# Kernel tuning notes

Measured on AMD Instinct MI355X. Metric: run time of the kernel, lower is better.

The kernel has to match this reference:

```python
import jax, jax.numpy as jnp
import numpy as np

EMBED_DIM = 1024
NUM_HEADS = 16
HEAD_DIM = EMBED_DIM // NUM_HEADS


def setup_inputs() -> dict:
    key = jax.random.key(0)
    ks = jax.random.split(key, 7)
    B, S, D = 2, 2048, EMBED_DIM
    s = 1.0 / np.sqrt(D)
    return {
        "x": jax.random.normal(ks[0], (B, S, D), dtype=jnp.float32),
        "Wq": jax.random.normal(ks[1], (D, D), dtype=jnp.float32) * s,
        "bq": jax.random.normal(ks[2], (D,), dtype=jnp.float32) * 0.01,
        "Wk": jax.random.normal(ks[3], (D, D), dtype=jnp.float32) * s,
        "bk": jax.random.normal(ks[4], (D,), dtype=jnp.float32) * 0.01,
        "Wv": jax.random.normal(ks[5], (D, D), dtype=jnp.float32) * s,
        "bv": jax.random.normal(ks[6], (D,), dtype=jnp.float32) * 0.01,
    }


def reference(x, Wq, bq, Wk, bk, Wv, bv):
    B, S, D = x.shape
    H, Hd = NUM_HEADS, HEAD_DIM
    # QKV projections, then split heads: [B, S, D] -> [B, H, S, Hd]
    q = (x @ Wq + bq).reshape(B, S, H, Hd).transpose(0, 2, 1, 3)
    k = (x @ Wk + bk).reshape(B, S, H, Hd).transpose(0, 2, 1, 3)
    v = (x @ Wv + bv).reshape(B, S, H, Hd).transpose(0, 2, 1, 3)
    # NOTE: the original module applies NO 1/sqrt(head_dim) scaling.
    energy = jnp.einsum("bhqd,bhkd->bhqk", q, k)  # [B, H, S, S]
    attn = jax.nn.softmax(energy, axis=-1)
    out = jnp.einsum("bhqk,bhkd->bhqd", attn, v)
    return out.transpose(0, 2, 1, 3).reshape(B, S, D)
```

## Files before the change

kernel.cpp:

```cpp
#include <hip/hip_runtime.h>
#include <stdint.h>
#include <stddef.h>

typedef _Float16 half_t;
typedef __attribute__((ext_vector_type(8))) _Float16 h16x8;
typedef __attribute__((ext_vector_type(4))) _Float16 h16x4;
typedef __attribute__((ext_vector_type(4))) float f32x4;

#define MFMA16(a, b, c) __builtin_amdgcn_mfma_f32_16x16x32_f16(a, b, c, 0, 0, 0)
#define EXP2(x) __builtin_amdgcn_exp2f(x)

#define SW(row, slot) ((((slot) ^ ((row) & 7))) * 8)

__device__ __forceinline__ void gload_lds16(const half_t* g, half_t* l) {
    __builtin_amdgcn_global_load_lds(
        (const __attribute__((address_space(1))) void*)g,
        (__attribute__((address_space(3))) void*)l, 16, 0, 0);
}

__global__ __launch_bounds__(256) void cvt_x_kernel(const float* __restrict__ x,
                                                    half_t* __restrict__ xh, int n8) {
    int i = blockIdx.x * blockDim.x + threadIdx.x;
    if (i >= n8) return;
    const float4* xv = (const float4*)x;
    float4 a = xv[i * 2 + 0];
    float4 b = xv[i * 2 + 1];
    h16x8 o;
    o[0] = (half_t)a.x; o[1] = (half_t)a.y; o[2] = (half_t)a.z; o[3] = (half_t)a.w;
    o[4] = (half_t)b.x; o[5] = (half_t)b.y; o[6] = (half_t)b.z; o[7] = (half_t)b.w;
    ((h16x8*)xh)[i] = o;
}

__global__ __launch_bounds__(256) void cvt_w_kernel(const float* __restrict__ Wq,
                                                    const float* __restrict__ Wk,
                                                    const float* __restrict__ Wv,
                                                    half_t* __restrict__ Wt) {
    __shared__ float t[32][33];
    const float* W = (blockIdx.z == 0) ? Wq : ((blockIdx.z == 1) ? Wk : Wv);
    int k0 = blockIdx.y * 32, n0 = blockIdx.x * 32;
    int tid = threadIdx.x;
    int r = tid >> 3;
    int c4 = (tid & 7) * 4;
    float4 v = *(const float4*)&W[(size_t)(k0 + r) * 1024 + n0 + c4];
    t[r][c4 + 0] = v.x; t[r][c4 + 1] = v.y; t[r][c4 + 2] = v.z; t[r][c4 + 3] = v.w;
    __syncthreads();
    half_t* o = Wt + (size_t)blockIdx.z * 1024 * 1024 + (size_t)(n0 + r) * 1024 + k0 + c4;
    h16x4 h;
    h[0] = (half_t)t[c4 + 0][r];
    h[1] = (half_t)t[c4 + 1][r];
    h[2] = (half_t)t[c4 + 2][r];
    h[3] = (half_t)t[c4 + 3][r];
    *(h16x4*)o = h;
}

__global__ __launch_bounds__(256, 3) void gemm_qkv_kernel(
    const half_t* __restrict__ xh,
    const half_t* __restrict__ Wt,
    const float* __restrict__ bq, const float* __restrict__ bk,
    const float* __restrict__ bv,
    half_t* __restrict__ qkv)
{
    const int p = blockIdx.z;
    const float* bias = (p == 0) ? bq : ((p == 1) ? bk : bv);
    const half_t* Wp = Wt + (size_t)p * 1024 * 1024;
    const int n0 = blockIdx.x * 128, m0 = blockIdx.y * 128;

    __shared__ half_t Al[128][64];
    __shared__ half_t Bl[128][64];

    const int tid = threadIdx.x;
    const int lane = tid & 63, wid = tid >> 6;
    const int wm = wid >> 1, wn = wid & 1;
    const int g = lane >> 4, r = lane & 15;

    const int lrow = lane >> 3;
    const int swzc = ((lane & 7) ^ lrow) * 8;

    f32x4 acc[4][4];
#pragma unroll
    for (int a = 0; a < 4; a++)
#pragma unroll
        for (int c = 0; c < 4; c++) acc[a][c] = (f32x4){0.f, 0.f, 0.f, 0.f};

    for (int k0 = 0; k0 < 1024; k0 += 64) {
        __syncthreads();
#pragma unroll
        for (int j = 0; j < 4; j++) {
            int issue = wid * 4 + j;
            int row = issue * 8 + lrow;
            gload_lds16(&xh[(size_t)(m0 + row) * 1024 + k0 + swzc], &Al[0][0] + issue * 512);
            gload_lds16(&Wp[(size_t)(n0 + row) * 1024 + k0 + swzc], &Bl[0][0] + issue * 512);
        }
        __syncthreads();

#pragma unroll
        for (int t = 0; t < 2; t++) {
            h16x8 af[4], bf[4];
#pragma unroll
            for (int mi = 0; mi < 4; mi++)
                af[mi] = *(const h16x8*)&Al[wm * 64 + mi * 16 + r][SW(r, t * 4 + g)];
#pragma unroll
            for (int ni = 0; ni < 4; ni++)
                bf[ni] = *(const h16x8*)&Bl[wn * 64 + ni * 16 + r][SW(r, t * 4 + g)];
#pragma unroll
            for (int mi = 0; mi < 4; mi++)
#pragma unroll
                for (int ni = 0; ni < 4; ni++)
                    acc[mi][ni] = MFMA16(af[mi], bf[ni], acc[mi][ni]);
        }
    }

    float bn[4];
#pragma unroll
    for (int ni = 0; ni < 4; ni++) bn[ni] = bias[n0 + wn * 64 + ni * 16 + r];

    if (p == 0) {
        half_t* outp = qkv;
#pragma unroll
        for (int mi = 0; mi < 4; mi++) {
#pragma unroll
            for (int ni = 0; ni < 4; ni++) {
                int n = n0 + wn * 64 + ni * 16 + r;
                int hq = n >> 6, hd = n & 63;
#pragma unroll
                for (int i = 0; i < 4; i++) {
                    int m = m0 + wm * 64 + mi * 16 + g * 4 + i;
                    int b = m >> 11, s = m & 2047;
                    outp[(((size_t)(b * 16 + hq) * 2048 + s) << 6) + hd] =
                        (half_t)(acc[mi][ni][i] + bn[ni]);
                }
            }
        }
    } else if (p == 1) {
        half_t* outp = qkv + (size_t)4194304;
        const int kt = ((m0 & 2047) + wm * 64) >> 6;
        const int bK = (m0 + wm * 64) >> 11;
#pragma unroll
        for (int ni = 0; ni < 4; ni++) {
            int n = n0 + wn * 64 + ni * 16 + r;
            int hK = n >> 6, hd = n & 63;
            int tt = hd >> 5, ggk = (hd >> 3) & 3, jK = hd & 7;
            size_t base = (size_t)(bK * 16 + hK) * 131072 + kt * 4096 + tt * 512 + ggk * 128 + jK;
#pragma unroll
            for (int mi = 0; mi < 4; mi++)
#pragma unroll
                for (int i = 0; i < 4; i++)
                    outp[base + mi * 1024 + (g * 4 + i) * 8] =
                        (half_t)(acc[mi][ni][i] + bn[ni]);
        }
    } else {
        half_t* outp = qkv + (size_t)2 * 4194304;
        const int kt = ((m0 & 2047) + wm * 64) >> 6;
        const int bV = (m0 + wm * 64) >> 11;
        const int hV = (n0 + wn * 64) >> 6;
        size_t base = (size_t)(bV * 16 + hV) * 131072 + kt * 4096 + (g * 16 + r) * 8;
#pragma unroll
        for (int ni = 0; ni < 4; ni++) {
#pragma unroll
            for (int mi = 0; mi < 4; mi++) {
                h16x4 pk;
#pragma unroll
                for (int i = 0; i < 4; i++) pk[i] = (half_t)(acc[mi][ni][i] + bn[ni]);
                *(h16x4*)&outp[base + (ni * 2 + (mi >> 1)) * 512 + (mi & 1) * 4] = pk;
            }
        }
    }
}

__global__ __launch_bounds__(256, 2) void attn_kernel(
    const half_t* __restrict__ Qg,
    const half_t* __restrict__ Kswz,
    const half_t* __restrict__ Vswz,
    float* __restrict__ out)
{
    const int tid = threadIdx.x;
    const int lane = tid & 63;
    const int g = lane >> 4, r = lane & 15;

    const int bid = blockIdx.x;
    const int xcd = bid & 7;
    const int t_  = bid >> 3;
    const int qblk = t_ & 15;
    const int bh = xcd + 8 * (t_ >> 4);

    const int b = bh >> 4, h = bh & 15;
    const half_t* Qb = Qg + (size_t)bh * 131072;
    const half_t* Kp = Kswz + (size_t)bh * 131072;
    const half_t* Vp = Vswz + (size_t)bh * 131072;
    const int q0 = qblk * 128 + (tid >> 6) * 32;
    const int lofs = g * 128 + r * 8;

    h16x8 qf[2][2];
#pragma unroll
    for (int qg = 0; qg < 2; qg++)
#pragma unroll
        for (int t = 0; t < 2; t++) {
            qf[qg][t] = *(const h16x8*)&Qb[(size_t)(q0 + qg * 16 + r) * 64 + t * 32 + g * 8];
            qf[qg][t] *= (half_t)1.44269504f;
        }

    const h16x8 ones8 = {(half_t)1.f, (half_t)1.f, (half_t)1.f, (half_t)1.f,
                         (half_t)1.f, (half_t)1.f, (half_t)1.f, (half_t)1.f};

    f32x4 o[2][4], lsum[2];
#pragma unroll
    for (int qg = 0; qg < 2; qg++) {
#pragma unroll
        for (int d = 0; d < 4; d++) o[qg][d] = (f32x4){0.f, 0.f, 0.f, 0.f};
        lsum[qg] = (f32x4){0.f, 0.f, 0.f, 0.f};
    }
    float m_run[2] = {0.f, 0.f};

    h16x8 kf[8], vf[8];

    auto loadK = [&](int kt) {
#pragma unroll
        for (int kc = 0; kc < 4; kc++)
#pragma unroll
            for (int t = 0; t < 2; t++)
                kf[kc * 2 + t] = *(const h16x8*)&Kp[kt * 4096 + kc * 1024 + t * 512 + lofs];
    };
    auto loadV = [&](int kt) {
#pragma unroll
        for (int dh = 0; dh < 8; dh++)
            vf[dh] = *(const h16x8*)&Vp[kt * 4096 + dh * 512 + lofs];
    };

    auto QKT = [&](f32x4 (&e)[2][4]) {
        __builtin_amdgcn_s_setprio(1);
#pragma unroll
        for (int kc = 0; kc < 4; kc++) {
            e[0][kc] = (f32x4){0.f, 0.f, 0.f, 0.f};
            e[1][kc] = (f32x4){0.f, 0.f, 0.f, 0.f};
#pragma unroll
            for (int t = 0; t < 2; t++) {
                e[0][kc] = MFMA16(kf[kc * 2 + t], qf[0][t], e[0][kc]);
                e[1][kc] = MFMA16(kf[kc * 2 + t], qf[1][t], e[1][kc]);
            }
        }
        __builtin_amdgcn_s_setprio(0);
    };

    auto SOFTMAX_PV = [&](f32x4 (&e)[2][4]) {
        h16x8 pa[2][2];
#pragma unroll
        for (int qg = 0; qg < 2; qg++) {
            float t0 = fmaxf(fmaxf(e[qg][0][0], e[qg][0][1]), e[qg][0][2]);
            float t1 = fmaxf(fmaxf(e[qg][0][3], e[qg][1][0]), e[qg][1][1]);
            float t2 = fmaxf(fmaxf(e[qg][1][2], e[qg][1][3]), e[qg][2][0]);
            float t3 = fmaxf(fmaxf(e[qg][2][1], e[qg][2][2]), e[qg][2][3]);
            float t4 = fmaxf(fmaxf(e[qg][3][0], e[qg][3][1]), e[qg][3][2]);
            float tm = fmaxf(fmaxf(t0, t1), fmaxf(fmaxf(t2, t3), fmaxf(t4, e[qg][3][3])));
            tm = fmaxf(tm, __shfl_xor(tm, 16));
            tm = fmaxf(tm, __shfl_xor(tm, 32));

#pragma unroll
            for (int kc = 0; kc < 4; kc++)
#pragma unroll
                for (int i = 0; i < 4; i++) e[qg][kc][i] = EXP2(e[qg][kc][i] - m_run[qg]);

            if (!__all(tm <= m_run[qg] + 8.f)) {
                float nm = fmaxf(m_run[qg], tm);
                float sc = EXP2(m_run[qg] - nm);
                m_run[qg] = nm;
#pragma unroll
                for (int kc = 0; kc < 4; kc++)
#pragma unroll
                    for (int i = 0; i < 4; i++) e[qg][kc][i] *= sc;
#pragma unroll
                for (int i = 0; i < 4; i++) {
                    float sci = __shfl(sc, (lane & 48) | (g * 4 + i));
                    lsum[qg][i] *= sci;
#pragma unroll
                    for (int d = 0; d < 4; d++) o[qg][d][i] *= sci;
                }
            }

#pragma unroll
            for (int ks = 0; ks < 2; ks++)
#pragma unroll
                for (int hf = 0; hf < 2; hf++)
#pragma unroll
                    for (int i = 0; i < 4; i++)
                        pa[qg][ks][hf * 4 + i] = (half_t)e[qg][ks * 2 + hf][i];
        }

        __builtin_amdgcn_s_setprio(1);
#pragma unroll
        for (int ks = 0; ks < 2; ks++) {
#pragma unroll
            for (int d = 0; d < 4; d++) {
                o[0][d] = MFMA16(pa[0][ks], vf[d * 2 + ks], o[0][d]);
                o[1][d] = MFMA16(pa[1][ks], vf[d * 2 + ks], o[1][d]);
            }
            lsum[0] = MFMA16(pa[0][ks], ones8, lsum[0]);
            lsum[1] = MFMA16(pa[1][ks], ones8, lsum[1]);
        }
        __builtin_amdgcn_s_setprio(0);
    };

    f32x4 eA[2][4], eB[2][4];
    loadK(0);
    QKT(eA);
    loadK(1);

    for (int kt = 0; kt < 32; kt += 2) {
        loadV(kt);
        QKT(eB);
        loadK((kt + 2) & 31);
        SOFTMAX_PV(eA);
        loadV(kt + 1);
        QKT(eA);
        loadK((kt + 3) & 31);
        SOFTMAX_PV(eB);
    }

#pragma unroll
    for (int qg = 0; qg < 2; qg++)
#pragma unroll
        for (int i = 0; i < 4; i++) {
            float inv = 1.0f / lsum[qg][i];
            int s = q0 + qg * 16 + g * 4 + i;
            float* op = out + (size_t)(b * 2048 + s) * 1024 + h * 64 + r;
#pragma unroll
            for (int d = 0; d < 4; d++) op[d * 16] = o[qg][d][i] * inv;
        }
}

extern "C" void kernel_launch(void* const* d_in, const int* in_sizes, int n_in,
                              void* d_out, int out_size, void* d_ws, size_t ws_size,
                              hipStream_t stream) {
    const float* x  = (const float*)d_in[0];
    const float* Wq = (const float*)d_in[1];
    const float* bq = (const float*)d_in[2];
    const float* Wk = (const float*)d_in[3];
    const float* bk = (const float*)d_in[4];
    const float* Wv = (const float*)d_in[5];
    const float* bv = (const float*)d_in[6];
    float* out = (float*)d_out;

    half_t* xh  = (half_t*)d_ws;
    half_t* Wt  = (half_t*)((char*)d_ws + (size_t)8 * 1024 * 1024);
    half_t* qkv = (half_t*)((char*)d_ws + (size_t)14 * 1024 * 1024);
    half_t* Qh  = qkv;
    half_t* Kh  = qkv + (size_t)4194304;
    half_t* Vth = qkv + (size_t)8388608;

    cvt_x_kernel<<<2048, 256, 0, stream>>>(x, xh, 524288);
    cvt_w_kernel<<<dim3(32, 32, 3), 256, 0, stream>>>(Wq, Wk, Wv, Wt);
    gemm_qkv_kernel<<<dim3(8, 32, 3), 256, 0, stream>>>(xh, Wt, bq, bk, bv, qkv);
    attn_kernel<<<512, 256, 0, stream>>>(Qh, Kh, Vth, out);
}
```

Baseline: 99.41 us.

## Halve per-wave query rows in attention and raise occupancy to four blocks

```diff
diff --git a/kernel.cpp b/kernel.cpp
--- a/kernel.cpp
+++ b/kernel.cpp
@@ -167,7 +167,7 @@
     }
 }
 
-__global__ __launch_bounds__(256, 2) void attn_kernel(
+__global__ __launch_bounds__(256, 4) void attn_kernel(
     const half_t* __restrict__ Qg,
     const half_t* __restrict__ Kswz,
     const half_t* __restrict__ Vswz,
@@ -180,36 +180,31 @@
     const int bid = blockIdx.x;
     const int xcd = bid & 7;
     const int t_  = bid >> 3;
-    const int qblk = t_ & 15;
-    const int bh = xcd + 8 * (t_ >> 4);
+    const int qblk = t_ & 31;
+    const int bh = xcd + 8 * (t_ >> 5);
 
     const int b = bh >> 4, h = bh & 15;
     const half_t* Qb = Qg + (size_t)bh * 131072;
     const half_t* Kp = Kswz + (size_t)bh * 131072;
     const half_t* Vp = Vswz + (size_t)bh * 131072;
-    const int q0 = qblk * 128 + (tid >> 6) * 32;
+    const int q0 = qblk * 64 + (tid >> 6) * 16;
     const int lofs = g * 128 + r * 8;
 
-    h16x8 qf[2][2];
-#pragma unroll
-    for (int qg = 0; qg < 2; qg++)
-#pragma unroll
-        for (int t = 0; t < 2; t++) {
-            qf[qg][t] = *(const h16x8*)&Qb[(size_t)(q0 + qg * 16 + r) * 64 + t * 32 + g * 8];
-            qf[qg][t] *= (half_t)1.44269504f;
-        }
+    h16x8 qf[2];
+#pragma unroll
+    for (int t = 0; t < 2; t++) {
+        qf[t] = *(const h16x8*)&Qb[(size_t)(q0 + r) * 64 + t * 32 + g * 8];
+        qf[t] *= (half_t)1.44269504f;
+    }
 
     const h16x8 ones8 = {(half_t)1.f, (half_t)1.f, (half_t)1.f, (half_t)1.f,
                          (half_t)1.f, (half_t)1.f, (half_t)1.f, (half_t)1.f};
 
-    f32x4 o[2][4], lsum[2];
-#pragma unroll
-    for (int qg = 0; qg < 2; qg++) {
-#pragma unroll
-        for (int d = 0; d < 4; d++) o[qg][d] = (f32x4){0.f, 0.f, 0.f, 0.f};
-        lsum[qg] = (f32x4){0.f, 0.f, 0.f, 0.f};
-    }
-    float m_run[2] = {0.f, 0.f};
+    f32x4 o[4], lsum;
+#pragma unroll
+    for (int d = 0; d < 4; d++) o[d] = (f32x4){0.f, 0.f, 0.f, 0.f};
+    lsum = (f32x4){0.f, 0.f, 0.f, 0.f};
+    float m_run = 0.f;
 
     h16x8 kf[8], vf[8];
 
@@ -226,105 +221,83 @@
             vf[dh] = *(const h16x8*)&Vp[kt * 4096 + dh * 512 + lofs];
     };
 
-    auto QKT = [&](f32x4 (&e)[2][4]) {
+    loadK(0);
+
+    for (int kt = 0; kt < 32; ++kt) {
+        loadV(kt);
+
+        f32x4 e[4];
         __builtin_amdgcn_s_setprio(1);
 #pragma unroll
         for (int kc = 0; kc < 4; kc++) {
-            e[0][kc] = (f32x4){0.f, 0.f, 0.f, 0.f};
-            e[1][kc] = (f32x4){0.f, 0.f, 0.f, 0.f};
-#pragma unroll
-            for (int t = 0; t < 2; t++) {
-                e[0][kc] = MFMA16(kf[kc * 2 + t], qf[0][t], e[0][kc]);
-                e[1][kc] = MFMA16(kf[kc * 2 + t], qf[1][t], e[1][kc]);
+            e[kc] = (f32x4){0.f, 0.f, 0.f, 0.f};
+#pragma unroll
+            for (int t = 0; t < 2; t++)
+                e[kc] = MFMA16(kf[kc * 2 + t], qf[t], e[kc]);
+        }
+        __builtin_amdgcn_s_setprio(0);
+
+        loadK((kt + 1) & 31);
+
+        float t0 = fmaxf(fmaxf(e[0][0], e[0][1]), e[0][2]);
+        float t1 = fmaxf(fmaxf(e[0][3], e[1][0]), e[1][1]);
+        float t2 = fmaxf(fmaxf(e[1][2], e[1][3]), e[2][0]);
+        float t3 = fmaxf(fmaxf(e[2][1], e[2][2]), e[2][3]);
+        float t4 = fmaxf(fmaxf(e[3][0], e[3][1]), e[3][2]);
+        float tm = fmaxf(fmaxf(t0, t1), fmaxf(fmaxf(t2, t3), fmaxf(t4, e[3][3])));
+        tm = fmaxf(tm, __shfl_xor(tm, 16));
+        tm = fmaxf(tm, __shfl_xor(tm, 32));
+
+#pragma unroll
+        for (int kc = 0; kc < 4; kc++)
+#pragma unroll
+            for (int i = 0; i < 4; i++) e[kc][i] = EXP2(e[kc][i] - m_run);
+
+        if (!__all(tm <= m_run + 8.f)) {
+            float nm = fmaxf(m_run, tm);
+            float sc = EXP2(m_run - nm);
+            m_run = nm;
+#pragma unroll
+            for (int kc = 0; kc < 4; kc++)
+#pragma unroll
+                for (int i = 0; i < 4; i++) e[kc][i] *= sc;
+#pragma unroll
+            for (int i = 0; i < 4; i++) {
+                float sci = __shfl(sc, (lane & 48) | (g * 4 + i));
+                lsum[i] *= sci;
+#pragma unroll
+                for (int d = 0; d < 4; d++) o[d][i] *= sci;
             }
         }
+
+        h16x8 pa[2];
+#pragma unroll
+        for (int ks = 0; ks < 2; ks++)
+#pragma unroll
+            for (int hf = 0; hf < 2; hf++)
+#pragma unroll
+                for (int i = 0; i < 4; i++)
+                    pa[ks][hf * 4 + i] = (half_t)e[ks * 2 + hf][i];
+
+        __builtin_amdgcn_s_setprio(1);
+#pragma unroll
+        for (int ks = 0; ks < 2; ks++) {
+#pragma unroll
+            for (int d = 0; d < 4; d++)
+                o[d] = MFMA16(pa[ks], vf[d * 2 + ks], o[d]);
+            lsum = MFMA16(pa[ks], ones8, lsum);
+        }
         __builtin_amdgcn_s_setprio(0);
-    };
-
-    auto SOFTMAX_PV = [&](f32x4 (&e)[2][4]) {
-        h16x8 pa[2][2];
-#pragma unroll
-        for (int qg = 0; qg < 2; qg++) {
-            float t0 = fmaxf(fmaxf(e[qg][0][0], e[qg][0][1]), e[qg][0][2]);
-            float t1 = fmaxf(fmaxf(e[qg][0][3], e[qg][1][0]), e[qg][1][1]);
-            float t2 = fmaxf(fmaxf(e[qg][1][2], e[qg][1][3]), e[qg][2][0]);
-            float t3 = fmaxf(fmaxf(e[qg][2][1], e[qg][2][2]), e[qg][2][3]);
-            float t4 = fmaxf(fmaxf(e[qg][3][0], e[qg][3][1]), e[qg][3][2]);
-            float tm = fmaxf(fmaxf(t0, t1), fmaxf(fmaxf(t2, t3), fmaxf(t4, e[qg][3][3])));
-            tm = fmaxf(tm, __shfl_xor(tm, 16));
-            tm = fmaxf(tm, __shfl_xor(tm, 32));
-
-#pragma unroll
-            for (int kc = 0; kc < 4; kc++)
-#pragma unroll
-                for (int i = 0; i < 4; i++) e[qg][kc][i] = EXP2(e[qg][kc][i] - m_run[qg]);
-
-            if (!__all(tm <= m_run[qg] + 8.f)) {
-                float nm = fmaxf(m_run[qg], tm);
-                float sc = EXP2(m_run[qg] - nm);
-                m_run[qg] = nm;
-#pragma unroll
-                for (int kc = 0; kc < 4; kc++)
-#pragma unroll
-                    for (int i = 0; i < 4; i++) e[qg][kc][i] *= sc;
-#pragma unroll
-                for (int i = 0; i < 4; i++) {
-                    float sci = __shfl(sc, (lane & 48) | (g * 4 + i));
-                    lsum[qg][i] *= sci;
-#pragma unroll
-                    for (int d = 0; d < 4; d++) o[qg][d][i] *= sci;
-                }
-            }
-
-#pragma unroll
-            for (int ks = 0; ks < 2; ks++)
-#pragma unroll
-                for (int hf = 0; hf < 2; hf++)
-#pragma unroll
-                    for (int i = 0; i < 4; i++)
-                        pa[qg][ks][hf * 4 + i] = (half_t)e[qg][ks * 2 + hf][i];
-        }
-
-        __builtin_amdgcn_s_setprio(1);
-#pragma unroll
-        for (int ks = 0; ks < 2; ks++) {
-#pragma unroll
-            for (int d = 0; d < 4; d++) {
-                o[0][d] = MFMA16(pa[0][ks], vf[d * 2 + ks], o[0][d]);
-                o[1][d] = MFMA16(pa[1][ks], vf[d * 2 + ks], o[1][d]);
-            }
-            lsum[0] = MFMA16(pa[0][ks], ones8, lsum[0]);
-            lsum[1] = MFMA16(pa[1][ks], ones8, lsum[1]);
-        }
-        __builtin_amdgcn_s_setprio(0);
-    };
-
-    f32x4 eA[2][4], eB[2][4];
-    loadK(0);
-    QKT(eA);
-    loadK(1);
-
-    for (int kt = 0; kt < 32; kt += 2) {
-        loadV(kt);
-        QKT(eB);
-        loadK((kt + 2) & 31);
-        SOFTMAX_PV(eA);
-        loadV(kt + 1);
-        QKT(eA);
-        loadK((kt + 3) & 31);
-        SOFTMAX_PV(eB);
-    }
-
-#pragma unroll
-    for (int qg = 0; qg < 2; qg++)
-#pragma unroll
-        for (int i = 0; i < 4; i++) {
-            float inv = 1.0f / lsum[qg][i];
-            int s = q0 + qg * 16 + g * 4 + i;
-            float* op = out + (size_t)(b * 2048 + s) * 1024 + h * 64 + r;
-#pragma unroll
-            for (int d = 0; d < 4; d++) op[d * 16] = o[qg][d][i] * inv;
-        }
+    }
+
+#pragma unroll
+    for (int i = 0; i < 4; i++) {
+        float inv = 1.0f / lsum[i];
+        int s = q0 + g * 4 + i;
+        float* op = out + (size_t)(b * 2048 + s) * 1024 + h * 64 + r;
+#pragma unroll
+        for (int d = 0; d < 4; d++) op[d * 16] = o[d][i] * inv;
+    }
 }
 
 extern "C" void kernel_launch(void* const* d_in, const int* in_sizes, int n_in,
@@ -349,5 +322,5 @@
     cvt_x_kernel<<<2048, 256, 0, stream>>>(x, xh, 524288);
     cvt_w_kernel<<<dim3(32, 32, 3), 256, 0, stream>>>(Wq, Wk, Wv, Wt);
     gemm_qkv_kernel<<<dim3(8, 32, 3), 256, 0, stream>>>(xh, Wt, bq, bk, bv, qkv);
-    attn_kernel<<<512, 256, 0, stream>>>(Qh, Kh, Vth, out);
-}
+    attn_kernel<<<1024, 256, 0, stream>>>(Qh, Kh, Vth, out);
+}
```

Result: slower. 120.4 us (+21.1%).
